# Kernel tuning notes

Measured on AMD Instinct MI355X. Metric: run time of the kernel, lower is better.

## Reference

```python
import jax, jax.numpy as jnp
import numpy as np

POOL = 7              # pool_size -> output resolution
H, W, C = 200, 304, 256   # stride-16 feature map of a ~3200x4864 image
N = 2000              # number of RoIs


def setup_inputs() -> dict:
    key = jax.random.key(0)
    k1, k2, k3 = jax.random.split(key, 3)
    fmap = jax.random.normal(k1, (1, H, W, C), dtype=jnp.float32)
    # rois are (x0, y0, x1, y1) in IMAGE pixel coords; forward divides by stride.
    stride = 16
    xy0 = jax.random.uniform(k2, (N, 2), dtype=jnp.float32) * jnp.array([W * stride * 0.6, H * stride * 0.6], jnp.float32)
    wh = jax.random.uniform(k3, (N, 2), dtype=jnp.float32, minval=0.05, maxval=0.4) * jnp.array([W * stride * 0.4, H * stride * 0.4], jnp.float32)
    rois = jnp.concatenate([xy0, xy0 + wh], axis=1)
    return {"shared_layers": fmap, "rois": rois, "extractor_stride": 16}


def _roi_align(fmap, boxes, resolution):
    """fmap: [1,H,W,C]; boxes: [N,4] (x0,y0,x1,y1) fp-coords on the feature map.
    Replicates crop_and_resize(pad_border=True) at 2x resolution + 2x2 avg pool,
    then NCHW transpose + flatten, exactly as the TF module."""
    img = jnp.pad(fmap[0], ((1, 1), (1, 1), (0, 0)), mode="symmetric")  # [H+2, W+2, C]
    boxes = jax.lax.stop_gradient(boxes) + 1.0  # account for 1-pixel symmetric pad
    Hp, Wp, Cc = img.shape
    n = boxes.shape[0]
    S = resolution * 2
    x0, y0, x1, y1 = boxes[:, 0], boxes[:, 1], boxes[:, 2], boxes[:, 3]
    sw = (x1 - x0) / S
    sh = (y1 - y0) / S
    i = jnp.arange(S, dtype=jnp.float32)
    # fpcoor sample centers: x0 + spacing/2 - 0.5 + i*spacing (== TF transform_fpcoor_for_tf grid)
    ys = y0[:, None] + sh[:, None] * (i + 0.5) - 0.5  # [N,S]
    xs = x0[:, None] + sw[:, None] * (i + 0.5) - 0.5  # [N,S]

    def idx(coords, size):
        f0 = jnp.floor(coords)
        frac = coords - f0
        i0 = jnp.clip(f0.astype(jnp.int32), 0, size - 1)
        i1 = jnp.clip(i0 + 1, 0, size - 1)
        valid = (coords >= 0) & (coords <= size - 1)  # TF extrapolation_value = 0
        return i0, i1, frac, valid

    yi0, yi1, ly, vy = idx(ys, Hp)
    xi0, xi1, lx, vx = idx(xs, Wp)

    g = lambda yi, xi: img[yi[:, :, None], xi[:, None, :]]  # gather -> [N,S,S,C]
    ly_, lx_ = ly[:, :, None, None], lx[:, None, :, None]
    crop = ((1.0 - ly_) * ((1.0 - lx_) * g(yi0, xi0) + lx_ * g(yi0, xi1))
            + ly_ * ((1.0 - lx_) * g(yi1, xi0) + lx_ * g(yi1, xi1)))
    crop = crop * (vy[:, :, None] & vx[:, None, :])[..., None].astype(crop.dtype)
    # 2x2 avg pool over spatial dims -> [N,res,res,C]
    pooled = crop.reshape(n, resolution, 2, resolution, 2, Cc).mean(axis=(2, 4))
    # transpose([0,3,1,2]) to NCHW then Flatten -> [N, C*res*res]
    return pooled.transpose(0, 3, 1, 2).reshape(n, -1)


def reference(shared_layers, rois, extractor_stride):
    boxes = rois / jnp.float32(extractor_stride)  # feature-map fp-coords
    return _roi_align(shared_layers, boxes, POOL)
```

## Files before the change

kernel.cpp:

```cpp
#include <hip/hip_runtime.h>


#define HH 200
#define WW 304
#define CC 256
#define HP (HH + 2)
#define WP (WW + 2)
#define PS 14
#define NCELL 49
#define LDS_STRIDE 257
#define NBUCKET 256

__global__ __launch_bounds__(256) void roi_sort_kernel(
    const float* __restrict__ rois,
    const int*   __restrict__ stride_p,
    int n, int* __restrict__ perm)
{
    __shared__ int hist[NBUCKET];
    __shared__ int scan[NBUCKET];
    __shared__ int offs[NBUCKET];
    const int t = threadIdx.x;
    hist[t] = 0;
    __syncthreads();

    const float inv = 1.0f / (float)stride_p[0];
    auto key_of = [&](int i) -> int {
        const float cx = 0.5f * (rois[4 * i + 0] + rois[4 * i + 2]) * inv;
        const float cy = 0.5f * (rois[4 * i + 1] + rois[4 * i + 3]) * inv;
        int tx = (int)(cx * (16.0f / (float)WW));
        int ty = (int)(cy * (16.0f / (float)HH));
        tx = min(max(tx, 0), 15);
        ty = min(max(ty, 0), 15);
        int k = 0;
#pragma unroll
        for (int b = 0; b < 4; ++b)
            k |= (((tx >> b) & 1) << (2 * b)) | (((ty >> b) & 1) << (2 * b + 1));
        return k;
    };

    for (int i = t; i < n; i += 256) atomicAdd(&hist[key_of(i)], 1);
    __syncthreads();

    scan[t] = hist[t];
    __syncthreads();
    for (int d = 1; d < NBUCKET; d <<= 1) {
        const int x = (t >= d) ? scan[t - d] : 0;
        __syncthreads();
        scan[t] += x;
        __syncthreads();
    }
    offs[t] = scan[t] - hist[t];
    __syncthreads();

    for (int i = t; i < n; i += 256) {
        const int pos = atomicAdd(&offs[key_of(i)], 1);
        perm[pos] = i;
    }
}

__global__ __launch_bounds__(256) void roi_align_kernel(
    const float* __restrict__ fmap,
    const float* __restrict__ rois,
    const int*   __restrict__ stride_p,
    const int*   __restrict__ perm,
    int nwg,
    float*       __restrict__ out)
{
    __shared__ float pool[NCELL * LDS_STRIDE];
    __shared__ int   yo0[PS], yo1[PS], xo0[PS], xo1[PS];
    __shared__ float lyv[PS], vyv[PS], lxv[PS], vxv[PS];

    const int t = threadIdx.x;

    const int bid = blockIdx.x;
    const int q = nwg >> 3, rem = nwg & 7;
    const int xcd = bid & 7, idx8 = bid >> 3;
    const int swz = (xcd < rem ? xcd * (q + 1) : rem * (q + 1) + (xcd - rem) * q) + idx8;
    const int r = perm[swz];

    if (t < 2 * PS) {
        const bool isx = (t >= PS);
        const int  i   = isx ? (t - PS) : t;
        const float inv = 1.0f / (float)stride_p[0];
        const float a0 = rois[4 * r + (isx ? 0 : 1)] * inv + 1.0f;
        const float a1 = rois[4 * r + (isx ? 2 : 3)] * inv + 1.0f;
        const float sc = (a1 - a0) / (float)PS;
        const float coord = a0 + sc * ((float)i + 0.5f) - 0.5f;
        const int size = isx ? WP : HP;

        const float f0   = floorf(coord);
        const float frac = coord - f0;
        int i0 = (int)f0;
        i0 = min(max(i0, 0), size - 1);
        const int i1 = min(i0 + 1, size - 1);
        const float valid = (coord >= 0.0f && coord <= (float)(size - 1)) ? 1.0f : 0.0f;

        if (isx) {
            const int c0 = min(max(i0 - 1, 0), WW - 1);
            const int c1 = min(max(i1 - 1, 0), WW - 1);
            xo0[i] = c0 * CC;
            xo1[i] = c1 * CC;
            lxv[i] = frac;
            vxv[i] = valid;
        } else {
            const int r0 = min(max(i0 - 1, 0), HH - 1);
            const int r1 = min(max(i1 - 1, 0), HH - 1);
            yo0[i] = r0 * (WW * CC);
            yo1[i] = r1 * (WW * CC);
            lyv[i] = frac;
            vyv[i] = valid;
        }
    }
    __syncthreads();

    const int cg = t & 63;
    const int sq = t >> 6;
    const float4* __restrict__ f4 = reinterpret_cast<const float4*>(fmap);

    for (int ss = sq; ss < NCELL; ss += 8) {
        const int  s0   = ss;
        const bool has1 = (ss + 4) < NCELL;
        const int  s1   = has1 ? ss + 4 : ss;
        const int py0 = s0 / 7, px0 = s0 - py0 * 7;
        const int py1 = s1 / 7, px1 = s1 - py1 * 7;
        float4 acc0 = make_float4(0.f, 0.f, 0.f, 0.f);
        float4 acc1 = make_float4(0.f, 0.f, 0.f, 0.f);
#pragma unroll
        for (int dy = 0; dy < 2; ++dy) {
            const int iy0 = 2 * py0 + dy,      iy1 = 2 * py1 + dy;
            const float ly0 = lyv[iy0],        ly1 = lyv[iy1];
            const float vy0 = vyv[iy0],        vy1 = vyv[iy1];
            const int ya0 = yo0[iy0] >> 2,     ya1 = yo0[iy1] >> 2;
            const int yb0 = yo1[iy0] >> 2,     yb1 = yo1[iy1] >> 2;
#pragma unroll
            for (int dx = 0; dx < 2; ++dx) {
                const int ix0 = 2 * px0 + dx,  ix1 = 2 * px1 + dx;
                const float lx0 = lxv[ix0],    lx1 = lxv[ix1];
                const float vx0 = vxv[ix0],    vx1 = vxv[ix1];
                const int xa0 = xo0[ix0] >> 2, xa1 = xo0[ix1] >> 2;
                const int xb0 = xo1[ix0] >> 2, xb1 = xo1[ix1] >> 2;

                const float4 a00 = f4[ya0 + xa0 + cg];
                const float4 a01 = f4[ya0 + xb0 + cg];
                const float4 a10 = f4[yb0 + xa0 + cg];
                const float4 a11 = f4[yb0 + xb0 + cg];
                const float4 b00 = f4[ya1 + xa1 + cg];
                const float4 b01 = f4[ya1 + xb1 + cg];
                const float4 b10 = f4[yb1 + xa1 + cg];
                const float4 b11 = f4[yb1 + xb1 + cg];

                const float m0   = 0.25f * vy0 * vx0;
                const float w00a = m0 * (1.f - ly0) * (1.f - lx0);
                const float w01a = m0 * (1.f - ly0) * lx0;
                const float w10a = m0 * ly0 * (1.f - lx0);
                const float w11a = m0 * ly0 * lx0;
                const float m1   = 0.25f * vy1 * vx1;
                const float w00b = m1 * (1.f - ly1) * (1.f - lx1);
                const float w01b = m1 * (1.f - ly1) * lx1;
                const float w10b = m1 * ly1 * (1.f - lx1);
                const float w11b = m1 * ly1 * lx1;

                acc0.x += w00a * a00.x + w01a * a01.x + w10a * a10.x + w11a * a11.x;
                acc0.y += w00a * a00.y + w01a * a01.y + w10a * a10.y + w11a * a11.y;
                acc0.z += w00a * a00.z + w01a * a01.z + w10a * a10.z + w11a * a11.z;
                acc0.w += w00a * a00.w + w01a * a01.w + w10a * a10.w + w11a * a11.w;
                acc1.x += w00b * b00.x + w01b * b01.x + w10b * b10.x + w11b * b11.x;
                acc1.y += w00b * b00.y + w01b * b01.y + w10b * b10.y + w11b * b11.y;
                acc1.z += w00b * b00.z + w01b * b01.z + w10b * b10.z + w11b * b11.z;
                acc1.w += w00b * b00.w + w01b * b01.w + w10b * b10.w + w11b * b11.w;
            }
        }
        {
            float* d0 = &pool[s0 * LDS_STRIDE + 4 * cg];
            d0[0] = acc0.x; d0[1] = acc0.y; d0[2] = acc0.z; d0[3] = acc0.w;
        }
        if (has1) {
            float* d1 = &pool[s1 * LDS_STRIDE + 4 * cg];
            d1[0] = acc1.x; d1[1] = acc1.y; d1[2] = acc1.z; d1[3] = acc1.w;
        }
    }
    __syncthreads();

    const size_t base = (size_t)r * (CC * NCELL);
#pragma unroll 1
    for (int k = 0; k < NCELL; ++k) {
        const int idx = t + (k << 8);
        const int c  = idx / NCELL;
        const int sp = idx - c * NCELL;
        out[base + idx] = pool[sp * LDS_STRIDE + c];
    }
}

extern "C" void kernel_launch(void* const* d_in, const int* in_sizes, int n_in,
                              void* d_out, int out_size, void* d_ws, size_t ws_size,
                              hipStream_t stream) {
    const float* fmap = (const float*)d_in[0];
    const float* rois = (const float*)d_in[1];
    const int*   strd = (const int*)d_in[2];
    float*       out  = (float*)d_out;
    int*         perm = (int*)d_ws;
    const int n = in_sizes[1] / 4;

    roi_sort_kernel<<<1, 256, 0, stream>>>(rois, strd, n, perm);
    roi_align_kernel<<<n, 256, 0, stream>>>(fmap, rois, strd, perm, n, out);
}
```

Baseline: 204.7 us.

## Halve LDS staging buffer with two-phase pooling and precompute bilinear tables

Splits the 49 output cells into two phases of 25 and 24 rows so the LDS transpose buffer is about half its former size. The row stride is padded and each 32-column group is skewed by one to avoid bank conflicts. Per-sample bilinear weights and gather offsets are precomputed once into LDS tables rather than recomputed per thread, and launch bounds now request 4 blocks per CU. The aim is higher occupancy to hide gather latency. The cost is extra barriers, and output writes per phase are less contiguous (strided by 49 within each channel).

```diff
diff --git a/kernel.cpp b/kernel.cpp
--- a/kernel.cpp
+++ b/kernel.cpp
@@ -8,7 +8,8 @@
 #define WP (WW + 2)
 #define PS 14
 #define NCELL 49
-#define LDS_STRIDE 257
+#define PROWS 25
+#define PSTRIDE 289
 #define NBUCKET 256
 
 __global__ __launch_bounds__(256) void roi_sort_kernel(
@@ -58,7 +59,7 @@
     }
 }
 
-__global__ __launch_bounds__(256) void roi_align_kernel(
+__global__ __launch_bounds__(256, 4) void roi_align_kernel(
     const float* __restrict__ fmap,
     const float* __restrict__ rois,
     const int*   __restrict__ stride_p,
@@ -66,16 +67,18 @@
     int nwg,
     float*       __restrict__ out)
 {
-    __shared__ float pool[NCELL * LDS_STRIDE];
+    __shared__ float pool[PROWS * PSTRIDE];
+    __shared__ float wtab[NCELL * 16];
+    __shared__ int   otab[NCELL * 16];
     __shared__ int   yo0[PS], yo1[PS], xo0[PS], xo1[PS];
     __shared__ float lyv[PS], vyv[PS], lxv[PS], vxv[PS];
 
     const int t = threadIdx.x;
 
     const int bid = blockIdx.x;
-    const int q = nwg >> 3, rem = nwg & 7;
+    const int q8 = nwg >> 3, rem = nwg & 7;
     const int xcd = bid & 7, idx8 = bid >> 3;
-    const int swz = (xcd < rem ? xcd * (q + 1) : rem * (q + 1) + (xcd - rem) * q) + idx8;
+    const int swz = (xcd < rem ? xcd * (q8 + 1) : rem * (q8 + 1) + (xcd - rem) * q8) + idx8;
     const int r = perm[swz];
 
     if (t < 2 * PS) {
@@ -96,98 +99,115 @@
         const float valid = (coord >= 0.0f && coord <= (float)(size - 1)) ? 1.0f : 0.0f;
 
         if (isx) {
-            const int c0 = min(max(i0 - 1, 0), WW - 1);
-            const int c1 = min(max(i1 - 1, 0), WW - 1);
-            xo0[i] = c0 * CC;
-            xo1[i] = c1 * CC;
+            xo0[i] = min(max(i0 - 1, 0), WW - 1) * CC;
+            xo1[i] = min(max(i1 - 1, 0), WW - 1) * CC;
             lxv[i] = frac;
             vxv[i] = valid;
         } else {
-            const int r0 = min(max(i0 - 1, 0), HH - 1);
-            const int r1 = min(max(i1 - 1, 0), HH - 1);
-            yo0[i] = r0 * (WW * CC);
-            yo1[i] = r1 * (WW * CC);
+            yo0[i] = min(max(i0 - 1, 0), HH - 1) * (WW * CC);
+            yo1[i] = min(max(i1 - 1, 0), HH - 1) * (WW * CC);
             lyv[i] = frac;
             vyv[i] = valid;
         }
     }
     __syncthreads();
 
+    if (t < NCELL * 4) {
+        const int s  = t >> 2;
+        const int qq = t & 3;
+        const int dy = qq >> 1, dx = qq & 1;
+        const int py = s / 7, px = s - py * 7;
+        const int iy = 2 * py + dy, ix = 2 * px + dx;
+
+        const float ly = lyv[iy], vy = vyv[iy];
+        const float lx = lxv[ix], vx = vxv[ix];
+        const float m = 0.25f * vy * vx;
+
+        float4 w;
+        w.x = m * (1.f - ly) * (1.f - lx);
+        w.y = m * (1.f - ly) * lx;
+        w.z = m * ly * (1.f - lx);
+        w.w = m * ly * lx;
+        int4 o;
+        o.x = (yo0[iy] + xo0[ix]) >> 2;
+        o.y = (yo0[iy] + xo1[ix]) >> 2;
+        o.z = (yo1[iy] + xo0[ix]) >> 2;
+        o.w = (yo1[iy] + xo1[ix]) >> 2;
+
+        reinterpret_cast<float4*>(wtab)[t] = w;
+        reinterpret_cast<int4*>(otab)[t]   = o;
+    }
+    __syncthreads();
+
     const int cg = t & 63;
     const int sq = t >> 6;
     const float4* __restrict__ f4 = reinterpret_cast<const float4*>(fmap);
-
-    for (int ss = sq; ss < NCELL; ss += 8) {
-        const int  s0   = ss;
-        const bool has1 = (ss + 4) < NCELL;
-        const int  s1   = has1 ? ss + 4 : ss;
-        const int py0 = s0 / 7, px0 = s0 - py0 * 7;
-        const int py1 = s1 / 7, px1 = s1 - py1 * 7;
-        float4 acc0 = make_float4(0.f, 0.f, 0.f, 0.f);
-        float4 acc1 = make_float4(0.f, 0.f, 0.f, 0.f);
+    const float4* wt4 = reinterpret_cast<const float4*>(wtab);
+    const int4*   ot4 = reinterpret_cast<const int4*>(otab);
+    const size_t base = (size_t)r * (CC * NCELL);
+
+#pragma unroll 1
+    for (int phase = 0; phase < 2; ++phase) {
+        const int s_lo = phase ? PROWS : 0;
+        const int s_hi = phase ? NCELL : PROWS;
+        const int nrow = s_hi - s_lo;
+
+        for (int ss = s_lo + sq; ss < s_hi; ss += 8) {
+            const int  s0   = ss;
+            const bool has1 = (ss + 4) < s_hi;
+            const int  s1   = has1 ? ss + 4 : ss;
+            float4 acc0 = make_float4(0.f, 0.f, 0.f, 0.f);
+            float4 acc1 = make_float4(0.f, 0.f, 0.f, 0.f);
 #pragma unroll
-        for (int dy = 0; dy < 2; ++dy) {
-            const int iy0 = 2 * py0 + dy,      iy1 = 2 * py1 + dy;
-            const float ly0 = lyv[iy0],        ly1 = lyv[iy1];
-            const float vy0 = vyv[iy0],        vy1 = vyv[iy1];
-            const int ya0 = yo0[iy0] >> 2,     ya1 = yo0[iy1] >> 2;
-            const int yb0 = yo1[iy0] >> 2,     yb1 = yo1[iy1] >> 2;
-#pragma unroll
-            for (int dx = 0; dx < 2; ++dx) {
-                const int ix0 = 2 * px0 + dx,  ix1 = 2 * px1 + dx;
-                const float lx0 = lxv[ix0],    lx1 = lxv[ix1];
-                const float vx0 = vxv[ix0],    vx1 = vxv[ix1];
-                const int xa0 = xo0[ix0] >> 2, xa1 = xo0[ix1] >> 2;
-                const int xb0 = xo1[ix0] >> 2, xb1 = xo1[ix1] >> 2;
-
-                const float4 a00 = f4[ya0 + xa0 + cg];
-                const float4 a01 = f4[ya0 + xb0 + cg];
-                const float4 a10 = f4[yb0 + xa0 + cg];
-                const float4 a11 = f4[yb0 + xb0 + cg];
-                const float4 b00 = f4[ya1 + xa1 + cg];
-                const float4 b01 = f4[ya1 + xb1 + cg];
-                const float4 b10 = f4[yb1 + xa1 + cg];
-                const float4 b11 = f4[yb1 + xb1 + cg];
-
-                const float m0   = 0.25f * vy0 * vx0;
-                const float w00a = m0 * (1.f - ly0) * (1.f - lx0);
-                const float w01a = m0 * (1.f - ly0) * lx0;
-                const float w10a = m0 * ly0 * (1.f - lx0);
-                const float w11a = m0 * ly0 * lx0;
-                const float m1   = 0.25f * vy1 * vx1;
-                const float w00b = m1 * (1.f - ly1) * (1.f - lx1);
-                const float w01b = m1 * (1.f - ly1) * lx1;
-                const float w10b = m1 * ly1 * (1.f - lx1);
-                const float w11b = m1 * ly1 * lx1;
-
-                acc0.x += w00a * a00.x + w01a * a01.x + w10a * a10.x + w11a * a11.x;
-                acc0.y += w00a * a00.y + w01a * a01.y + w10a * a10.y + w11a * a11.y;
-                acc0.z += w00a * a00.z + w01a * a01.z + w10a * a10.z + w11a * a11.z;
-                acc0.w += w00a * a00.w + w01a * a01.w + w10a * a10.w + w11a * a11.w;
-                acc1.x += w00b * b00.x + w01b * b01.x + w10b * b10.x + w11b * b11.x;
-                acc1.y += w00b * b00.y + w01b * b01.y + w10b * b10.y + w11b * b11.y;
-                acc1.z += w00b * b00.z + w01b * b01.z + w10b * b10.z + w11b * b11.z;
-                acc1.w += w00b * b00.w + w01b * b01.w + w10b * b10.w + w11b * b11.w;
+            for (int qq = 0; qq < 4; ++qq) {
+                const float4 w0 = wt4[s0 * 4 + qq];
+                const int4   o0 = ot4[s0 * 4 + qq];
+                const float4 w1 = wt4[s1 * 4 + qq];
+                const int4   o1 = ot4[s1 * 4 + qq];
+
+                const float4 a0 = f4[o0.x + cg];
+                const float4 a1 = f4[o0.y + cg];
+                const float4 a2 = f4[o0.z + cg];
+                const float4 a3 = f4[o0.w + cg];
+                const float4 b0 = f4[o1.x + cg];
+                const float4 b1 = f4[o1.y + cg];
+                const float4 b2 = f4[o1.z + cg];
+                const float4 b3 = f4[o1.w + cg];
+
+                acc0.x += w0.x * a0.x + w0.y * a1.x + w0.z * a2.x + w0.w * a3.x;
+                acc0.y += w0.x * a0.y + w0.y * a1.y + w0.z * a2.y + w0.w * a3.y;
+                acc0.z += w0.x * a0.z + w0.y * a1.z + w0.z * a2.z + w0.w * a3.z;
+                acc0.w += w0.x * a0.w + w0.y * a1.w + w0.z * a2.w + w0.w * a3.w;
+                acc1.x += w1.x * b0.x + w1.y * b1.x + w1.z * b2.x + w1.w * b3.x;
+                acc1.y += w1.x * b0.y + w1.y * b1.y + w1.z * b2.y + w1.w * b3.y;
+                acc1.z += w1.x * b0.z + w1.y * b1.z + w1.z * b2.z + w1.w * b3.z;
+                acc1.w += w1.x * b0.w + w1.y * b1.w + w1.z * b2.w + w1.w * b3.w;
+            }
+            {
+                const int row = s0 - s_lo;
+                const int c0  = 4 * cg;
+                const int col = c0 + (c0 >> 5);
+                float* d0 = &pool[row * PSTRIDE + col];
+                d0[0] = acc0.x; d0[1] = acc0.y; d0[2] = acc0.z; d0[3] = acc0.w;
+            }
+            if (has1) {
+                const int row = s1 - s_lo;
+                const int c0  = 4 * cg;
+                const int col = c0 + (c0 >> 5);
+                float* d1 = &pool[row * PSTRIDE + col];
+                d1[0] = acc1.x; d1[1] = acc1.y; d1[2] = acc1.z; d1[3] = acc1.w;
             }
         }
-        {
-            float* d0 = &pool[s0 * LDS_STRIDE + 4 * cg];
-            d0[0] = acc0.x; d0[1] = acc0.y; d0[2] = acc0.z; d0[3] = acc0.w;
+        __syncthreads();
+
+        const int total = nrow * CC;
+#pragma unroll 1
+        for (int e = t; e < total; e += 256) {
+            const int c  = e / nrow;
+            const int sp = e - c * nrow;
+            out[base + c * NCELL + s_lo + sp] = pool[sp * PSTRIDE + c + (c >> 5)];
         }
-        if (has1) {
-            float* d1 = &pool[s1 * LDS_STRIDE + 4 * cg];
-            d1[0] = acc1.x; d1[1] = acc1.y; d1[2] = acc1.z; d1[3] = acc1.w;
-        }
-    }
-    __syncthreads();
-
-    const size_t base = (size_t)r * (CC * NCELL);
-#pragma unroll 1
-    for (int k = 0; k < NCELL; ++k) {
-        const int idx = t + (k << 8);
-        const int c  = idx / NCELL;
-        const int sp = idx - c * NCELL;
-        out[base + idx] = pool[sp * LDS_STRIDE + c];
+        __syncthreads();
     }
 }
 
```

Result: slower. 227.8 us (+11.3%).
